# Performance work log

Hardware: AMD Instinct MI355X
Metric: run time of the kernel (lower is better)

## Reference

```python
import jax, jax.numpy as jnp
import numpy as np

BETA = 5.5  # exp-cosine kernel sharpness (module default)

def _l2norm(x, axis=-1):
    return x / jnp.linalg.norm(x, axis=axis, keepdims=True)

def setup_inputs() -> dict:
    key = jax.random.key(0)
    ks = jax.random.split(key, 7)
    C, Mt, D = 1000, 33, 1024  # classes, memory slots (32 learned + 1 fixed), feat dim
    img_feat = jax.random.normal(ks[0], (1, D), jnp.float32)
    memory = jax.random.normal(ks[1], (C, Mt, D), jnp.float32)
    # simulate unfilled memory slots (exercises the zero-row masking branch)
    memory = memory.at[:, 24:32, :].set(0.0)
    global_bias = jax.random.normal(ks[2], (C, D), jnp.float32) * 0.02
    global_bias_key = jax.random.normal(ks[3], (C, D), jnp.float32) * 0.02
    global_bias_value = jax.random.normal(ks[4], (C, D), jnp.float32) * 0.02
    global_ffn_bias = jax.random.normal(ks[5], (C, D), jnp.float32) * 0.02
    logit_scale = jnp.ones((1,), jnp.float32) * jnp.log(100.0).astype(jnp.float32)
    return {
        "img_feat": img_feat,
        "memory": memory,
        "global_bias": global_bias,
        "global_bias_key": global_bias_key,
        "global_bias_value": global_bias_value,
        "global_ffn_bias": global_ffn_bias,
        "logit_scale": logit_scale,
    }

def reference(img_feat, memory, global_bias, global_bias_key, global_bias_value,
              global_ffn_bias, logit_scale):
    # position == 'all', center_type_clip == 'attn'
    # query: image feature shifted by mean class bias, L2-normalized
    q = _l2norm(img_feat + jnp.mean(global_bias, axis=0, keepdims=True))  # [1, D]
    # keys / values: per-class bias add + L2 norm, with empty slots zeroed
    empty = (jnp.sum(memory, axis=-1) == 0)[..., None]                    # [C, Mt, 1]
    K = jnp.where(empty, 0.0, _l2norm(memory + global_bias_key[:, None, :]))
    V = jnp.where(empty, 0.0, _l2norm(memory + global_bias_value[:, None, :]))
    # exp-cosine similarity kernel: exp(-beta * (1 - cos))
    sim = jnp.einsum('d,cmd->cm', q[0], K)                                # [C, Mt]
    sim = jnp.exp(-BETA * (1.0 - sim))
    # weighted sum over memory slots, renormalize, output bias, renormalize
    a = _l2norm(jnp.einsum('cm,cmd->cd', sim, V))                          # [C, D]
    a = _l2norm(a + global_ffn_bias)
    logits = jnp.exp(logit_scale[0]) * (a @ img_feat[0])                   # [C]
    return jax.nn.softmax(logits)[None, :]                                 # [1, C]
```

## Files before the change

### kernel.cpp

```cpp
#include <hip/hip_runtime.h>
#include <math.h>

#define NCLS 1000
#define MT 33
#define D 1024
#define BETA 5.5f

__device__ __forceinline__ float wave_sum(float v) {
#pragma unroll
  for (int off = 32; off; off >>= 1) v += __shfl_xor(v, off, 64);
  return v;
}

__device__ __forceinline__ float dot4(float4 a, float4 b) {
  return a.x * b.x + a.y * b.y + a.z * b.z + a.w * b.w;
}

__device__ __forceinline__ float block_sum16(float v, volatile float* scr) {
  v = wave_sum(v);
  const int wv = threadIdx.x >> 6, lane = threadIdx.x & 63;
  if (lane == 0) scr[wv] = v;
  __syncthreads();
  if (wv == 0) {
    float x = (lane < 16) ? scr[lane] : 0.0f;
#pragma unroll
    for (int off = 8; off; off >>= 1) x += __shfl_xor(x, off, 64);
    if (lane == 0) scr[16] = x;
  }
  __syncthreads();
  return scr[16];
}

__global__ __launch_bounds__(1024) void zero_kernel(float* __restrict__ s) {
  s[threadIdx.x] = 0.0f;
}

__global__ __launch_bounds__(1024) void colsum_kernel(const float* __restrict__ gb,
                                                      float* __restrict__ s) {
  const int t = threadIdx.x;
  float p = 0.0f;
  for (int c = blockIdx.x; c < NCLS; c += gridDim.x) p += gb[(size_t)c * D + t];
  atomicAdd(&s[t], p);
}

__global__ __launch_bounds__(256, 4) void main_kernel(
    const float* __restrict__ memp, const float* __restrict__ gbk,
    const float* __restrict__ gbv, const float* __restrict__ gffn,
    const float* __restrict__ img, const float* __restrict__ s,
    const float* __restrict__ ls, float* __restrict__ logits) {
  __shared__ float red[4][D];
  const int c = blockIdx.x;
  const int t = threadIdx.x;
  const int wv = t >> 6, lane = t & 63;
  const int dbase = lane * 4;

  const float* gbk_c = gbk + (size_t)c * D;
  const float* gbv_c = gbv + (size_t)c * D;

  float4 qv[4], kv[4], vvr[4];
  float qss = 0.0f;
#pragma unroll
  for (int k = 0; k < 4; ++k) {
    const int d = k * 256 + dbase;
    const float4 iv = *(const float4*)(img + d);
    const float4 sv = *(const float4*)(s + d);
    float4 v;
    v.x = iv.x + sv.x * (1.0f / (float)NCLS);
    v.y = iv.y + sv.y * (1.0f / (float)NCLS);
    v.z = iv.z + sv.z * (1.0f / (float)NCLS);
    v.w = iv.w + sv.w * (1.0f / (float)NCLS);
    qv[k] = v;
    qss += dot4(v, v);
    kv[k] = *(const float4*)(gbk_c + d);
    vvr[k] = *(const float4*)(gbv_c + d);
  }
  qss = wave_sum(qss);
  const float qinv = 1.0f / sqrtf(qss);
#pragma unroll
  for (int k = 0; k < 4; ++k) {
    qv[k].x *= qinv; qv[k].y *= qinv; qv[k].z *= qinv; qv[k].w *= qinv;
  }

  float kk = 0.0f, vv2 = 0.0f, qk = 0.0f;
#pragma unroll
  for (int k = 0; k < 4; ++k) {
    kk += dot4(kv[k], kv[k]);
    vv2 += dot4(vvr[k], vvr[k]);
    qk += dot4(qv[k], kv[k]);
  }
  kk = wave_sum(kk);
  vv2 = wave_sum(vv2);
  qk = wave_sum(qk);

  float4 acc[4];
#pragma unroll
  for (int k = 0; k < 4; ++k) acc[k] = make_float4(0.f, 0.f, 0.f, 0.f);
  float Wsum = 0.0f;

  const float* memc = memp + (size_t)c * MT * D;
  for (int m = wv; m < MT; m += 4) {
    float4 mv[4];
#pragma unroll
    for (int k = 0; k < 4; ++k)
      mv[k] = *(const float4*)(memc + (size_t)m * D + k * 256 + dbase);
    float pqm = 0.f, pkm = 0.f, pvm = 0.f, pmm = 0.f;
#pragma unroll
    for (int k = 0; k < 4; ++k) {
      pqm += dot4(qv[k], mv[k]);
      pkm += dot4(kv[k], mv[k]);
      pvm += dot4(vvr[k], mv[k]);
      pmm += dot4(mv[k], mv[k]);
    }
    pqm = wave_sum(pqm);
    pkm = wave_sum(pkm);
    pvm = wave_sum(pvm);
    pmm = wave_sum(pmm);

    const float nk = sqrtf(pmm + 2.0f * pkm + kk);
    const float cosv = (pqm + qk) / nk;
    const float sim = expf(-BETA * (1.0f - cosv));
    const float nv = sqrtf(pmm + 2.0f * pvm + vv2);
    const float wgt = (pmm == 0.0f) ? 0.0f : sim / nv;
    Wsum += wgt;
#pragma unroll
    for (int k = 0; k < 4; ++k) {
      acc[k].x += wgt * mv[k].x;
      acc[k].y += wgt * mv[k].y;
      acc[k].z += wgt * mv[k].z;
      acc[k].w += wgt * mv[k].w;
    }
  }
#pragma unroll
  for (int k = 0; k < 4; ++k) {
    acc[k].x += Wsum * vvr[k].x;
    acc[k].y += Wsum * vvr[k].y;
    acc[k].z += Wsum * vvr[k].z;
    acc[k].w += Wsum * vvr[k].w;
  }

#pragma unroll
  for (int k = 0; k < 4; ++k) *(float4*)(&red[wv][k * 256 + dbase]) = acc[k];
  __syncthreads();
#pragma unroll
  for (int k = 0; k < 4; ++k) {
    const float4 a0 = *(const float4*)(&red[0][k * 256 + dbase]);
    const float4 a1 = *(const float4*)(&red[1][k * 256 + dbase]);
    const float4 a2 = *(const float4*)(&red[2][k * 256 + dbase]);
    const float4 a3 = *(const float4*)(&red[3][k * 256 + dbase]);
    acc[k].x = a0.x + a1.x + a2.x + a3.x;
    acc[k].y = a0.y + a1.y + a2.y + a3.y;
    acc[k].z = a0.z + a1.z + a2.z + a3.z;
    acc[k].w = a0.w + a1.w + a2.w + a3.w;
  }

  float n1 = 0.0f;
#pragma unroll
  for (int k = 0; k < 4; ++k) n1 += dot4(acc[k], acc[k]);
  n1 = wave_sum(n1);
  const float inv1 = 1.0f / sqrtf(n1);

  const float* gffn_c = gffn + (size_t)c * D;
  float n2 = 0.0f, d3 = 0.0f;
#pragma unroll
  for (int k = 0; k < 4; ++k) {
    const int d = k * 256 + dbase;
    const float4 gf = *(const float4*)(gffn_c + d);
    const float4 iv = *(const float4*)(img + d);
    float4 a1v;
    a1v.x = acc[k].x * inv1 + gf.x;
    a1v.y = acc[k].y * inv1 + gf.y;
    a1v.z = acc[k].z * inv1 + gf.z;
    a1v.w = acc[k].w * inv1 + gf.w;
    n2 += dot4(a1v, a1v);
    d3 += dot4(a1v, iv);
  }
  n2 = wave_sum(n2);
  d3 = wave_sum(d3);
  if (t == 0) logits[c] = expf(ls[0]) * d3 / sqrtf(n2);
}

__global__ __launch_bounds__(1024) void softmax_kernel(const float* __restrict__ logits,
                                                       float* __restrict__ out) {
  __shared__ float scr[40];
  const int t = threadIdx.x;
  const int wv = t >> 6, lane = t & 63;
  const float l = (t < NCLS) ? logits[t] : -INFINITY;
  float m = l;
#pragma unroll
  for (int off = 32; off; off >>= 1) m = fmaxf(m, __shfl_xor(m, off, 64));
  if (lane == 0) scr[wv] = m;
  __syncthreads();
  if (wv == 0) {
    float x = (lane < 16) ? scr[lane] : -INFINITY;
#pragma unroll
    for (int off = 8; off; off >>= 1) x = fmaxf(x, __shfl_xor(x, off, 64));
    if (lane == 0) scr[16] = x;
  }
  __syncthreads();
  m = scr[16];
  const float e = (t < NCLS) ? expf(l - m) : 0.0f;
  const float sden = block_sum16(e, scr);
  if (t < NCLS) out[t] = e / sden;
}

extern "C" void kernel_launch(void* const* d_in, const int* in_sizes, int n_in,
                              void* d_out, int out_size, void* d_ws, size_t ws_size,
                              hipStream_t stream) {
  const float* img = (const float*)d_in[0];
  const float* memp = (const float*)d_in[1];
  const float* gb = (const float*)d_in[2];
  const float* gbk = (const float*)d_in[3];
  const float* gbv = (const float*)d_in[4];
  const float* gffn = (const float*)d_in[5];
  const float* ls = (const float*)d_in[6];
  float* out = (float*)d_out;

  float* s = (float*)d_ws;
  float* logits = s + D;

  zero_kernel<<<1, D, 0, stream>>>(s);
  colsum_kernel<<<64, D, 0, stream>>>(gb, s);
  main_kernel<<<NCLS, 256, 0, stream>>>(memp, gbk, gbv, gffn, img, s, ls, logits);
  softmax_kernel<<<1, D, 0, stream>>>(logits, out);
}
```

Before: 229.9 us.

## Fuse softmax into main kernel via last-block atomic counter and prefetch memory rows

Removes the separate softmax launch. Each block now bumps a global atomic counter after writing its logit, and the last block to finish computes the softmax over all 1000 logits. The memory-row loop also software-prefetches the next slot's row into registers while the current one is processed, to hide load latency. This adds a threadfence and an atomic per block, serialises the softmax tail onto one 256-thread block, and raises register pressure.

Measured after the change: 266.4 us. 15.9% more time.

```diff
diff --git a/kernel.cpp b/kernel.cpp
--- a/kernel.cpp
+++ b/kernel.cpp
@@ -12,27 +12,20 @@
   return v;
 }
 
+__device__ __forceinline__ float wave_max(float v) {
+#pragma unroll
+  for (int off = 32; off; off >>= 1) v = fmaxf(v, __shfl_xor(v, off, 64));
+  return v;
+}
+
 __device__ __forceinline__ float dot4(float4 a, float4 b) {
   return a.x * b.x + a.y * b.y + a.z * b.z + a.w * b.w;
 }
 
-__device__ __forceinline__ float block_sum16(float v, volatile float* scr) {
-  v = wave_sum(v);
-  const int wv = threadIdx.x >> 6, lane = threadIdx.x & 63;
-  if (lane == 0) scr[wv] = v;
-  __syncthreads();
-  if (wv == 0) {
-    float x = (lane < 16) ? scr[lane] : 0.0f;
-#pragma unroll
-    for (int off = 8; off; off >>= 1) x += __shfl_xor(x, off, 64);
-    if (lane == 0) scr[16] = x;
-  }
-  __syncthreads();
-  return scr[16];
-}
-
-__global__ __launch_bounds__(1024) void zero_kernel(float* __restrict__ s) {
+__global__ __launch_bounds__(1024) void zero_kernel(float* __restrict__ s,
+                                                    unsigned* __restrict__ cnt) {
   s[threadIdx.x] = 0.0f;
+  if (threadIdx.x == 0) *cnt = 0u;
 }
 
 __global__ __launch_bounds__(1024) void colsum_kernel(const float* __restrict__ gb,
@@ -47,8 +40,10 @@
     const float* __restrict__ memp, const float* __restrict__ gbk,
     const float* __restrict__ gbv, const float* __restrict__ gffn,
     const float* __restrict__ img, const float* __restrict__ s,
-    const float* __restrict__ ls, float* __restrict__ logits) {
+    const float* __restrict__ ls, float* __restrict__ logits,
+    unsigned* __restrict__ cnt, float* __restrict__ out) {
   __shared__ float red[4][D];
+  __shared__ int winner_flag;
   const int c = blockIdx.x;
   const int t = threadIdx.x;
   const int wv = t >> 6, lane = t & 63;
@@ -98,11 +93,21 @@
   float Wsum = 0.0f;
 
   const float* memc = memp + (size_t)c * MT * D;
-  for (int m = wv; m < MT; m += 4) {
-    float4 mv[4];
-#pragma unroll
-    for (int k = 0; k < 4; ++k)
-      mv[k] = *(const float4*)(memc + (size_t)m * D + k * 256 + dbase);
+  int m = wv;
+  float4 mv[4];
+  {
+    const float* rp = memc + (size_t)m * D + dbase;
+#pragma unroll
+    for (int k = 0; k < 4; ++k) mv[k] = *(const float4*)(rp + k * 256);
+  }
+  while (m < MT) {
+    const int mn = m + 4;
+    float4 nx[4];
+    if (mn < MT) {
+      const float* np = memc + (size_t)mn * D + dbase;
+#pragma unroll
+      for (int k = 0; k < 4; ++k) nx[k] = *(const float4*)(np + k * 256);
+    }
     float pqm = 0.f, pkm = 0.f, pvm = 0.f, pmm = 0.f;
 #pragma unroll
     for (int k = 0; k < 4; ++k) {
@@ -129,6 +134,9 @@
       acc[k].z += wgt * mv[k].z;
       acc[k].w += wgt * mv[k].w;
     }
+#pragma unroll
+    for (int k = 0; k < 4; ++k) mv[k] = nx[k];
+    m = mn;
   }
 #pragma unroll
   for (int k = 0; k < 4; ++k) {
@@ -176,31 +184,44 @@
   }
   n2 = wave_sum(n2);
   d3 = wave_sum(d3);
-  if (t == 0) logits[c] = expf(ls[0]) * d3 / sqrtf(n2);
-}
-
-__global__ __launch_bounds__(1024) void softmax_kernel(const float* __restrict__ logits,
-                                                       float* __restrict__ out) {
-  __shared__ float scr[40];
-  const int t = threadIdx.x;
-  const int wv = t >> 6, lane = t & 63;
-  const float l = (t < NCLS) ? logits[t] : -INFINITY;
-  float m = l;
-#pragma unroll
-  for (int off = 32; off; off >>= 1) m = fmaxf(m, __shfl_xor(m, off, 64));
-  if (lane == 0) scr[wv] = m;
+
+  if (t == 0) {
+    logits[c] = expf(ls[0]) * d3 / sqrtf(n2);
+    __threadfence();
+    const unsigned old = atomicAdd(cnt, 1u);
+    winner_flag = (old == NCLS - 1) ? 1 : 0;
+  }
   __syncthreads();
-  if (wv == 0) {
-    float x = (lane < 16) ? scr[lane] : -INFINITY;
-#pragma unroll
-    for (int off = 8; off; off >>= 1) x = fmaxf(x, __shfl_xor(x, off, 64));
-    if (lane == 0) scr[16] = x;
-  }
-  __syncthreads();
-  m = scr[16];
-  const float e = (t < NCLS) ? expf(l - m) : 0.0f;
-  const float sden = block_sum16(e, scr);
-  if (t < NCLS) out[t] = e / sden;
+  if (winner_flag) {
+    __threadfence();
+    const int i4 = t * 4;
+    float4 lv = make_float4(-INFINITY, -INFINITY, -INFINITY, -INFINITY);
+    if (i4 < NCLS) lv = *(const float4*)(logits + i4);
+    float mloc = fmaxf(fmaxf(lv.x, lv.y), fmaxf(lv.z, lv.w));
+    mloc = wave_max(mloc);
+    if (lane == 0) red[0][wv] = mloc;
+    __syncthreads();
+    const float mall = fmaxf(fmaxf(red[0][0], red[0][1]), fmaxf(red[0][2], red[0][3]));
+    float4 ev = make_float4(0.f, 0.f, 0.f, 0.f);
+    if (i4 < NCLS) {
+      ev.x = expf(lv.x - mall);
+      ev.y = expf(lv.y - mall);
+      ev.z = expf(lv.z - mall);
+      ev.w = expf(lv.w - mall);
+    }
+    float sloc = wave_sum(ev.x + ev.y + ev.z + ev.w);
+    if (lane == 0) red[1][wv] = sloc;
+    __syncthreads();
+    const float inv_s = 1.0f / (red[1][0] + red[1][1] + red[1][2] + red[1][3]);
+    if (i4 < NCLS) {
+      float4 o;
+      o.x = ev.x * inv_s;
+      o.y = ev.y * inv_s;
+      o.z = ev.z * inv_s;
+      o.w = ev.w * inv_s;
+      *(float4*)(out + i4) = o;
+    }
+  }
 }
 
 extern "C" void kernel_launch(void* const* d_in, const int* in_sizes, int n_in,
@@ -217,9 +238,10 @@
 
   float* s = (float*)d_ws;
   float* logits = s + D;
-
-  zero_kernel<<<1, D, 0, stream>>>(s);
+  unsigned* cnt = (unsigned*)(s + 2 * D + 1024);
+
+  zero_kernel<<<1, D, 0, stream>>>(s, cnt);
   colsum_kernel<<<64, D, 0, stream>>>(gb, s);
-  main_kernel<<<NCLS, 256, 0, stream>>>(memp, gbk, gbv, gffn, img, s, ls, logits);
-  softmax_kernel<<<1, D, 0, stream>>>(logits, out);
-}
+  main_kernel<<<NCLS, 256, 0, stream>>>(memp, gbk, gbv, gffn, img, s, ls, logits,
+                                        cnt, out);
+}
```
